# Performance work log

Measured on AMD Instinct MI355X. Metric: run time of the kernel, lower is better.

The kernel has to match this reference:

```python
import jax, jax.numpy as jnp
import numpy as np

N_NODES = 50000
N_EDGES = 800000
IN_DIM, HID, OUT = 128, 64, 64
NUM_REL = 2
LN_EPS = 1e-5


def setup_inputs() -> dict:
    key = jax.random.key(0)
    ks = jax.random.split(key, 16)
    inp = {
        "x": jax.random.normal(ks[0], (N_NODES, IN_DIM), dtype=jnp.float32),
        "edge_index": jax.random.randint(ks[1], (2, N_EDGES), 0, N_NODES, dtype=jnp.int64),
        "edge_type": jax.random.randint(ks[2], (N_EDGES,), 0, NUM_REL, dtype=jnp.int64),
        # layer 1 params (RGCNConv input->hidden + LayerNorm)
        "W1": jax.random.normal(ks[3], (NUM_REL, IN_DIM, HID), dtype=jnp.float32) * 0.05,
        "root1": jax.random.normal(ks[4], (IN_DIM, HID), dtype=jnp.float32) * 0.05,
        "b1": jnp.zeros((HID,), dtype=jnp.float32),
        "g1": jnp.ones((HID,), dtype=jnp.float32),
        "beta1": jnp.zeros((HID,), dtype=jnp.float32),
        # layer 2 params (RGCNConv hidden->output + LayerNorm)
        "W2": jax.random.normal(ks[5], (NUM_REL, HID, OUT), dtype=jnp.float32) * 0.05,
        "root2": jax.random.normal(ks[6], (HID, OUT), dtype=jnp.float32) * 0.05,
        "b2": jnp.zeros((OUT,), dtype=jnp.float32),
        "g2": jnp.ones((OUT,), dtype=jnp.float32),
        "beta2": jnp.zeros((OUT,), dtype=jnp.float32),
    }
    return inp


def rgcn_conv(x, W, root, bias, src, dst, edge_type, num_nodes):
    # PyG RGCNConv (aggr='mean'): out = x @ root + bias + sum_r mean_{j in N_r(i)} x_j @ W_r
    out = x @ root + bias
    for r in range(NUM_REL):
        mask = (edge_type == r).astype(x.dtype)        # [E]
        proj = x @ W[r]                                 # [N, out]
        msg = proj[src] * mask[:, None]                 # [E, out] gather + mask
        agg = jax.ops.segment_sum(msg, dst, num_segments=num_nodes)   # scatter-add
        cnt = jax.ops.segment_sum(mask, dst, num_segments=num_nodes)  # per-relation in-degree
        out = out + agg / jnp.maximum(cnt, 1.0)[:, None]
    return out


def layer_norm(x, g, b):
    mu = jnp.mean(x, axis=-1, keepdims=True)
    var = jnp.mean(jnp.square(x - mu), axis=-1, keepdims=True)
    return (x - mu) * jax.lax.rsqrt(var + LN_EPS) * g + b


def reference(x, edge_index, edge_type, W1, root1, b1, g1, beta1, W2, root2, b2, g2, beta2):
    src, dst = edge_index[0], edge_index[1]
    h = rgcn_conv(x, W1, root1, b1, src, dst, edge_type, x.shape[0])
    h = layer_norm(h, g1, beta1)
    h = jax.nn.gelu(h, approximate=False)  # dropout is identity in eval mode
    h = rgcn_conv(h, W2, root2, b2, src, dst, edge_type, x.shape[0])
    h = layer_norm(h, g2, beta2)
    return h
```

## Files before the change

### kernel.cpp

```cpp
#include <hip/hip_runtime.h>
#include <hip/hip_bf16.h>
#include <math.h>

#define IN_DIM 128
#define HID 64
#define NREL 2

using f32x4 = __attribute__((ext_vector_type(4))) float;
using s16x8 = __attribute__((ext_vector_type(8))) short;

__device__ __forceinline__ short f2bf(float f) {
    unsigned u = __float_as_uint(f);
    unsigned r = (u + 0x7fffu + ((u >> 16) & 1u)) >> 16;
    return (short)r;
}
__device__ __forceinline__ float bf2f(short b) {
    return __uint_as_float(((unsigned)(unsigned short)b) << 16);
}

__global__ void zero_ints(int* p, int n) {
    int i = blockIdx.x * blockDim.x + threadIdx.x;
    if (i < n) p[i] = 0;
}

__global__ void count_edges(const int* __restrict__ et, const int* __restrict__ dst,
                            int* __restrict__ cnt, int E, int N) {
    int e = blockIdx.x * blockDim.x + threadIdx.x;
    if (e < E) {
        atomicAdd(&cnt[et[e] * N + dst[e]], 1);
    }
}

#define SCAN_T 256
#define SCAN_I 4
__global__ void scan_phase1(const int* __restrict__ in, const int* __restrict__ in2,
                            int* __restrict__ excl, int* __restrict__ bsum, int n) {
    __shared__ int sdata[SCAN_T];
    int b = blockIdx.x;
    int t = threadIdx.x;
    int base = b * SCAN_T * SCAN_I;
    int v[SCAN_I];
    int s = 0;
#pragma unroll
    for (int i = 0; i < SCAN_I; ++i) {
        int idx = base + t * SCAN_I + i;
        v[i] = (idx < n) ? (in2 ? in[idx] + in2[idx] : in[idx]) : 0;
        s += v[i];
    }
    sdata[t] = s;
    __syncthreads();
    for (int off = 1; off < SCAN_T; off <<= 1) {
        int x = (t >= off) ? sdata[t - off] : 0;
        __syncthreads();
        sdata[t] += x;
        __syncthreads();
    }
    int run = sdata[t] - s;
    if (bsum && t == SCAN_T - 1) bsum[b] = sdata[SCAN_T - 1];
#pragma unroll
    for (int i = 0; i < SCAN_I; ++i) {
        int idx = base + t * SCAN_I + i;
        if (idx < n) excl[idx] = run;
        run += v[i];
    }
}

__global__ void scan_phase3(const int* __restrict__ excl, const int* __restrict__ boff,
                            int* __restrict__ rowptr, int* __restrict__ cursor,
                            int n, int total) {
    int i = blockIdx.x * blockDim.x + threadIdx.x;
    if (i < n) {
        int v = excl[i] + boff[i / (SCAN_T * SCAN_I)];
        rowptr[i] = v;
        cursor[i] = v;
    }
    if (i == 0) rowptr[n] = total;
}

__global__ void fill_edges(const int* __restrict__ et, const int* __restrict__ src,
                           const int* __restrict__ dst, const int* __restrict__ cnt2,
                           int* __restrict__ cursor, int2* __restrict__ colw,
                           int E, int N) {
    int e = blockIdx.x * blockDim.x + threadIdx.x;
    if (e < E) {
        int d = dst[e];
        int r = et[e];
        int s = src[e];
        int slot = atomicAdd(&cursor[d], 1);
        int deg = cnt2[r * N + d];
        float iw = 1.f / (float)deg;
        unsigned long long v = (unsigned long long)(unsigned)(r * N + s) |
                               ((unsigned long long)__float_as_uint(iw) << 32);
        __hip_atomic_store((unsigned long long*)(colw + slot), v,
                           __ATOMIC_RELAXED, __HIP_MEMORY_SCOPE_AGENT);
    }
}

__device__ __forceinline__ void repack_one(const float* Wa, const float* Wb,
                                           const float* Wr, short* Wf, int T,
                                           int idx) {
    int g = idx >> 9;
    int r = idx & 511;
    int lane = r >> 3;
    int j = r & 7;
    int part = g & 1;
    int ct = g >> 1;
    int t = ct % T;
    int c = ct / T;
    int col = c * 16 + (lane & 15);
    int k = t * 32 + ((lane >> 4) << 3) + j;
    const float* Wg = (col < 64) ? Wa : (col < 128) ? Wb : Wr;
    float v = Wg[(size_t)k * 64 + (col & 63)];
    short hi = f2bf(v);
    Wf[idx] = part ? f2bf(v - bf2f(hi)) : hi;
}

__global__ void repack_w_frag(const float* __restrict__ W1,
                              const float* __restrict__ root1,
                              const float* __restrict__ W2,
                              const float* __restrict__ root2,
                              short* __restrict__ Wf1, short* __restrict__ Wf2) {
    const int L1 = 12 * 4 * 2 * 512;
    const int L2 = 12 * 2 * 2 * 512;
    int tid = blockIdx.x * blockDim.x + threadIdx.x;
    if (tid < L1) {
        repack_one(W1, W1 + (size_t)IN_DIM * 64, root1, Wf1, 4, tid);
    } else if (tid < L1 + L2) {
        repack_one(W2, W2 + (size_t)HID * 64, root2, Wf2, 2, tid - L1);
    }
}

template <int K>
__global__ __launch_bounds__(256) void gemm_mfma(
    const float* __restrict__ X, const short* __restrict__ Wf,
    float* __restrict__ PA, float* __restrict__ PB, float* __restrict__ PR,
    int M) {
    constexpr int T = K / 32;
    const int lane = threadIdx.x & 63;
    const int wid = threadIdx.x >> 6;
    const int row0 = blockIdx.x * 32 + (wid >> 1) * 16;
    const int cbase = (wid & 1) * 6;

    int arow = row0 + (lane & 15);
    if (arow > M - 1) arow = M - 1;
    const float* xr = X + (size_t)arow * K + ((lane >> 4) << 3);
    const s16x8* WfV = (const s16x8*)Wf;

    float4 xa[T][2];
#pragma unroll
    for (int t = 0; t < T; ++t) {
        xa[t][0] = *reinterpret_cast<const float4*>(xr + t * 32);
        xa[t][1] = *reinterpret_cast<const float4*>(xr + t * 32 + 4);
    }
    s16x8 ah[T], al[T];
#pragma unroll
    for (int t = 0; t < T; ++t) {
        const float av[8] = {xa[t][0].x, xa[t][0].y, xa[t][0].z, xa[t][0].w,
                             xa[t][1].x, xa[t][1].y, xa[t][1].z, xa[t][1].w};
#pragma unroll
        for (int j = 0; j < 8; ++j) {
            short h = f2bf(av[j]);
            ah[t][j] = h;
            al[t][j] = f2bf(av[j] - bf2f(h));
        }
    }

    f32x4 acc[6];
#pragma unroll
    for (int c = 0; c < 6; ++c) acc[c] = (f32x4){0.f, 0.f, 0.f, 0.f};

    s16x8 bhA[T], blA[T], bhB[T], blB[T];

#define LOADB(H, L, CG)                                                       \
    {                                                                         \
        _Pragma("unroll") for (int t = 0; t < T; ++t) {                       \
            H[t] = WfV[(size_t)(((CG) * T + t) * 2 + 0) * 64 + lane];         \
            L[t] = WfV[(size_t)(((CG) * T + t) * 2 + 1) * 64 + lane];         \
        }                                                                     \
    }
#define DOMFMA(H, L, CI)                                                      \
    {                                                                         \
        _Pragma("unroll") for (int t = 0; t < T; ++t) {                       \
            acc[CI] = __builtin_amdgcn_mfma_f32_16x16x32_bf16(ah[t], H[t],    \
                                                              acc[CI], 0, 0, 0); \
            acc[CI] = __builtin_amdgcn_mfma_f32_16x16x32_bf16(al[t], H[t],    \
                                                              acc[CI], 0, 0, 0); \
            acc[CI] = __builtin_amdgcn_mfma_f32_16x16x32_bf16(ah[t], L[t],    \
                                                              acc[CI], 0, 0, 0); \
        }                                                                     \
    }

    LOADB(bhA, blA, cbase + 0);
    LOADB(bhB, blB, cbase + 1);
    DOMFMA(bhA, blA, 0);
    LOADB(bhA, blA, cbase + 2);
    DOMFMA(bhB, blB, 1);
    LOADB(bhB, blB, cbase + 3);
    DOMFMA(bhA, blA, 2);
    LOADB(bhA, blA, cbase + 4);
    DOMFMA(bhB, blB, 3);
    LOADB(bhB, blB, cbase + 5);
    DOMFMA(bhA, blA, 4);
    DOMFMA(bhB, blB, 5);

#undef LOADB
#undef DOMFMA

    const int drow = row0 + ((lane >> 4) << 2);
    const int dcol = lane & 15;
#pragma unroll
    for (int ci = 0; ci < 6; ++ci) {
        const int cg = cbase + ci;
        float* base = (cg < 4) ? PA : (cg < 8) ? PB : PR;
        const int cc = (cg & 3) * 16 + dcol;
#pragma unroll
        for (int q = 0; q < 4; ++q) {
            const int row = drow + q;
            if (row < M) base[(size_t)row * 64 + cc] = acc[ci][q];
        }
    }
}

__device__ __forceinline__ float4 shfl_xor_f4(float4 v, int m) {
    return make_float4(__shfl_xor(v.x, m), __shfl_xor(v.y, m),
                       __shfl_xor(v.z, m), __shfl_xor(v.w, m));
}

__global__ __launch_bounds__(256) void agg_ln_kernel(
    const float* __restrict__ Pcat,
    const float* __restrict__ PR,
    const int* __restrict__ rowptr,
    const int2* __restrict__ colw,
    const float* __restrict__ bias, const float* __restrict__ g,
    const float* __restrict__ beta,
    float* __restrict__ out, int N, int gelu) {
    const int t = threadIdx.x;
    const int lane = t & 63;
    const int sub = lane >> 4;
    const int c = lane & 15;
    const int node = blockIdx.x * 4 + (t >> 6);
    if (node >= N) return;

    const int c4 = c * 4;
    float4 acc = *reinterpret_cast<const float4*>(PR + (size_t)node * 64 + c4);
    {
        float4 b4 = *reinterpret_cast<const float4*>(bias + c4);
        acc.x += b4.x; acc.y += b4.y; acc.z += b4.z; acc.w += b4.w;
    }

    const int beg = rowptr[node];
    const int end = rowptr[node + 1];
    float4 s0 = make_float4(0.f, 0.f, 0.f, 0.f);
    float4 s1 = s0, s2 = s0, s3 = s0;
    for (int i = beg + sub; i < end; i += 16) {
        {
            const int2 w = colw[i];
            const float4 v = *reinterpret_cast<const float4*>(Pcat + w.x * 64 + c4);
            const float f = __int_as_float(w.y);
            s0.x = fmaf(v.x, f, s0.x); s0.y = fmaf(v.y, f, s0.y);
            s0.z = fmaf(v.z, f, s0.z); s0.w = fmaf(v.w, f, s0.w);
        }
        int j = i + 4;
        if (j < end) {
            const int2 w = colw[j];
            const float4 v = *reinterpret_cast<const float4*>(Pcat + w.x * 64 + c4);
            const float f = __int_as_float(w.y);
            s1.x = fmaf(v.x, f, s1.x); s1.y = fmaf(v.y, f, s1.y);
            s1.z = fmaf(v.z, f, s1.z); s1.w = fmaf(v.w, f, s1.w);
        }
        j = i + 8;
        if (j < end) {
            const int2 w = colw[j];
            const float4 v = *reinterpret_cast<const float4*>(Pcat + w.x * 64 + c4);
            const float f = __int_as_float(w.y);
            s2.x = fmaf(v.x, f, s2.x); s2.y = fmaf(v.y, f, s2.y);
            s2.z = fmaf(v.z, f, s2.z); s2.w = fmaf(v.w, f, s2.w);
        }
        j = i + 12;
        if (j < end) {
            const int2 w = colw[j];
            const float4 v = *reinterpret_cast<const float4*>(Pcat + w.x * 64 + c4);
            const float f = __int_as_float(w.y);
            s3.x = fmaf(v.x, f, s3.x); s3.y = fmaf(v.y, f, s3.y);
            s3.z = fmaf(v.z, f, s3.z); s3.w = fmaf(v.w, f, s3.w);
        }
    }
    s0.x += s1.x + s2.x + s3.x;
    s0.y += s1.y + s2.y + s3.y;
    s0.z += s1.z + s2.z + s3.z;
    s0.w += s1.w + s2.w + s3.w;
    float4 o = shfl_xor_f4(s0, 16);
    s0.x += o.x; s0.y += o.y; s0.z += o.z; s0.w += o.w;
    o = shfl_xor_f4(s0, 32);
    s0.x += o.x; s0.y += o.y; s0.z += o.z; s0.w += o.w;
    acc.x += s0.x; acc.y += s0.y; acc.z += s0.z; acc.w += s0.w;

    float ps = acc.x + acc.y + acc.z + acc.w;
#pragma unroll
    for (int off = 1; off <= 8; off <<= 1) ps += __shfl_xor(ps, off);
    const float mu = ps * (1.f / 64.f);
    const float4 d = make_float4(acc.x - mu, acc.y - mu, acc.z - mu, acc.w - mu);
    float vs = d.x * d.x + d.y * d.y + d.z * d.z + d.w * d.w;
#pragma unroll
    for (int off = 1; off <= 8; off <<= 1) vs += __shfl_xor(vs, off);
    const float rstd = 1.f / sqrtf(vs * (1.f / 64.f) + 1e-5f);

    const float4 g4 = *reinterpret_cast<const float4*>(g + c4);
    const float4 be4 = *reinterpret_cast<const float4*>(beta + c4);
    float4 y;
    y.x = d.x * rstd * g4.x + be4.x;
    y.y = d.y * rstd * g4.y + be4.y;
    y.z = d.z * rstd * g4.z + be4.z;
    y.w = d.w * rstd * g4.w + be4.w;

    if (gelu) {
        y.x = 0.5f * y.x * (1.f + erff(y.x * 0.70710678118654752440f));
        y.y = 0.5f * y.y * (1.f + erff(y.y * 0.70710678118654752440f));
        y.z = 0.5f * y.z * (1.f + erff(y.z * 0.70710678118654752440f));
        y.w = 0.5f * y.w * (1.f + erff(y.w * 0.70710678118654752440f));
    }

    if (sub == 0)
        *reinterpret_cast<float4*>(out + (size_t)node * 64 + c4) = y;
}

extern "C" void kernel_launch(void* const* d_in, const int* in_sizes, int n_in,
                              void* d_out, int out_size, void* d_ws, size_t ws_size,
                              hipStream_t stream) {
    const float* x = (const float*)d_in[0];
    const int* ei = (const int*)d_in[1];
    const int* et = (const int*)d_in[2];
    const float* W1 = (const float*)d_in[3];
    const float* root1 = (const float*)d_in[4];
    const float* b1 = (const float*)d_in[5];
    const float* g1 = (const float*)d_in[6];
    const float* beta1 = (const float*)d_in[7];
    const float* W2 = (const float*)d_in[8];
    const float* root2 = (const float*)d_in[9];
    const float* b2 = (const float*)d_in[10];
    const float* g2 = (const float*)d_in[11];
    const float* beta2 = (const float*)d_in[12];

    const int E = in_sizes[2];
    const int N = in_sizes[0] / IN_DIM;

    const int WF1 = 12 * 4 * 2 * 512;
    const int WF2 = 12 * 2 * 2 * 512;

    short* Wf1 = (short*)d_ws;
    short* Wf2 = Wf1 + WF1;
    float* Pcat = (float*)(Wf2 + WF2);
    float* PR   = Pcat + (size_t)2 * N * 64;
    float* H    = PR + (size_t)N * 64;
    int2* colw  = (int2*)(H + (size_t)N * 64);
    int* cnt2   = (int*)(colw + E);
    int* excl   = cnt2 + 2 * N;
    int* rowptr = excl + N;
    int* cursor = rowptr + N + 1;
    int* bsum   = cursor + N;
    int* boff   = bsum + 256;

    const int* esrc = ei;
    const int* edst = ei + E;

    zero_ints<<<(2 * N + 255) / 256, 256, 0, stream>>>(cnt2, 2 * N);
    count_edges<<<(E + 255) / 256, 256, 0, stream>>>(et, edst, cnt2, E, N);
    int nb = (N + SCAN_T * SCAN_I - 1) / (SCAN_T * SCAN_I);
    scan_phase1<<<nb, SCAN_T, 0, stream>>>(cnt2, cnt2 + N, excl, bsum, N);
    scan_phase1<<<1, SCAN_T, 0, stream>>>(bsum, nullptr, boff, nullptr, nb);
    scan_phase3<<<(N + 255) / 256, 256, 0, stream>>>(excl, boff, rowptr, cursor, N, E);
    fill_edges<<<(E + 255) / 256, 256, 0, stream>>>(et, esrc, edst, cnt2, cursor,
                                                    colw, E, N);

    repack_w_frag<<<(WF1 + WF2 + 255) / 256, 256, 0, stream>>>(
        W1, root1, W2, root2, Wf1, Wf2);

    int gblocks = (N + 31) / 32;
    gemm_mfma<IN_DIM><<<gblocks, 256, 0, stream>>>(
        x, Wf1, Pcat, Pcat + (size_t)N * 64, PR, N);
    agg_ln_kernel<<<(N + 3) / 4, 256, 0, stream>>>(Pcat, PR, rowptr, colw, b1, g1,
                                                   beta1, H, N, 1);

    gemm_mfma<HID><<<gblocks, 256, 0, stream>>>(
        H, Wf2, Pcat, Pcat + (size_t)N * 64, PR, N);
    agg_ln_kernel<<<(N + 3) / 4, 256, 0, stream>>>(Pcat, PR, rowptr, colw, b2, g2,
                                                   beta2, (float*)d_out, N, 0);
}
```

Measured before the change: 290.3 us.

## Stage weight fragments in LDS and give each wave all 12 output column groups

The GEMM kernel now loads the pre-packed bf16 weight fragments into shared memory in two K-phases. Each wave computes a 16-row tile across all 12 column groups, so each block covers 64 rows instead of 32. Previously each wave read its 6 column groups directly from global memory. The aim is to cut repeated global/L2 weight traffic and halve the block count. In exchange it uses more accumulator registers (12 f32x4), adds LDS staging with barriers, and sets a launch_bounds occupancy hint of 3.

Result: no change. 289.4 us (-0.3%).

```diff
diff --git a/kernel.cpp b/kernel.cpp
--- a/kernel.cpp
+++ b/kernel.cpp
@@ -131,15 +131,18 @@
 }
 
 template <int K>
-__global__ __launch_bounds__(256) void gemm_mfma(
+__global__ __launch_bounds__(256, 3) void gemm_mfma(
     const float* __restrict__ X, const short* __restrict__ Wf,
     float* __restrict__ PA, float* __restrict__ PB, float* __restrict__ PR,
     int M) {
     constexpr int T = K / 32;
-    const int lane = threadIdx.x & 63;
-    const int wid = threadIdx.x >> 6;
-    const int row0 = blockIdx.x * 32 + (wid >> 1) * 16;
-    const int cbase = (wid & 1) * 6;
+    constexpr int TH = T / 2;
+    __shared__ s16x8 WfL[12 * TH * 2 * 64];
+
+    const int tid = threadIdx.x;
+    const int lane = tid & 63;
+    const int wid = tid >> 6;
+    const int row0 = blockIdx.x * 64 + wid * 16;
 
     int arow = row0 + (lane & 15);
     if (arow > M - 1) arow = M - 1;
@@ -165,58 +168,53 @@
         }
     }
 
-    f32x4 acc[6];
-#pragma unroll
-    for (int c = 0; c < 6; ++c) acc[c] = (f32x4){0.f, 0.f, 0.f, 0.f};
-
-    s16x8 bhA[T], blA[T], bhB[T], blB[T];
-
-#define LOADB(H, L, CG)                                                       \
-    {                                                                         \
-        _Pragma("unroll") for (int t = 0; t < T; ++t) {                       \
-            H[t] = WfV[(size_t)(((CG) * T + t) * 2 + 0) * 64 + lane];         \
-            L[t] = WfV[(size_t)(((CG) * T + t) * 2 + 1) * 64 + lane];         \
-        }                                                                     \
-    }
-#define DOMFMA(H, L, CI)                                                      \
-    {                                                                         \
-        _Pragma("unroll") for (int t = 0; t < T; ++t) {                       \
-            acc[CI] = __builtin_amdgcn_mfma_f32_16x16x32_bf16(ah[t], H[t],    \
-                                                              acc[CI], 0, 0, 0); \
-            acc[CI] = __builtin_amdgcn_mfma_f32_16x16x32_bf16(al[t], H[t],    \
-                                                              acc[CI], 0, 0, 0); \
-            acc[CI] = __builtin_amdgcn_mfma_f32_16x16x32_bf16(ah[t], L[t],    \
-                                                              acc[CI], 0, 0, 0); \
-        }                                                                     \
-    }
-
-    LOADB(bhA, blA, cbase + 0);
-    LOADB(bhB, blB, cbase + 1);
-    DOMFMA(bhA, blA, 0);
-    LOADB(bhA, blA, cbase + 2);
-    DOMFMA(bhB, blB, 1);
-    LOADB(bhB, blB, cbase + 3);
-    DOMFMA(bhA, blA, 2);
-    LOADB(bhA, blA, cbase + 4);
-    DOMFMA(bhB, blB, 3);
-    LOADB(bhB, blB, cbase + 5);
-    DOMFMA(bhA, blA, 4);
-    DOMFMA(bhB, blB, 5);
-
-#undef LOADB
-#undef DOMFMA
+    f32x4 acc[12];
+#pragma unroll
+    for (int c = 0; c < 12; ++c) acc[c] = (f32x4){0.f, 0.f, 0.f, 0.f};
+
+#pragma unroll
+    for (int ph = 0; ph < 2; ++ph) {
+        if (ph) __syncthreads();
+#pragma unroll
+        for (int it = 0; it < (12 * TH * 2 * 64) / 256; ++it) {
+            const int v = it * 256 + tid;
+            const int chunk = v >> 6;
+            const int i = v & 63;
+            const int c = chunk / (TH * 2);
+            const int rem = chunk - c * (TH * 2);
+            const int tl = rem >> 1;
+            const int part = rem & 1;
+            const int gsrc = (c * T + ph * TH + tl) * 2 + part;
+            WfL[v] = WfV[(size_t)gsrc * 64 + i];
+        }
+        __syncthreads();
+#pragma unroll
+        for (int c = 0; c < 12; ++c) {
+#pragma unroll
+            for (int tl = 0; tl < TH; ++tl) {
+                const s16x8 bh = WfL[((c * TH + tl) * 2 + 0) * 64 + lane];
+                const s16x8 bl = WfL[((c * TH + tl) * 2 + 1) * 64 + lane];
+                const int tg = ph * TH + tl;
+                acc[c] = __builtin_amdgcn_mfma_f32_16x16x32_bf16(ah[tg], bh,
+                                                                 acc[c], 0, 0, 0);
+                acc[c] = __builtin_amdgcn_mfma_f32_16x16x32_bf16(al[tg], bh,
+                                                                 acc[c], 0, 0, 0);
+                acc[c] = __builtin_amdgcn_mfma_f32_16x16x32_bf16(ah[tg], bl,
+                                                                 acc[c], 0, 0, 0);
+            }
+        }
+    }
 
     const int drow = row0 + ((lane >> 4) << 2);
     const int dcol = lane & 15;
 #pragma unroll
-    for (int ci = 0; ci < 6; ++ci) {
-        const int cg = cbase + ci;
+    for (int cg = 0; cg < 12; ++cg) {
         float* base = (cg < 4) ? PA : (cg < 8) ? PB : PR;
         const int cc = (cg & 3) * 16 + dcol;
 #pragma unroll
         for (int q = 0; q < 4; ++q) {
             const int row = drow + q;
-            if (row < M) base[(size_t)row * 64 + cc] = acc[ci][q];
+            if (row < M) base[(size_t)row * 64 + cc] = acc[cg][q];
         }
     }
 }
@@ -375,7 +373,7 @@
     repack_w_frag<<<(WF1 + WF2 + 255) / 256, 256, 0, stream>>>(
         W1, root1, W2, root2, Wf1, Wf2);
 
-    int gblocks = (N + 31) / 32;
+    int gblocks = (N + 63) / 64;
     gemm_mfma<IN_DIM><<<gblocks, 256, 0, stream>>>(
         x, Wf1, Pcat, Pcat + (size_t)N * 64, PR, N);
     agg_ln_kernel<<<(N + 3) / 4, 256, 0, stream>>>(Pcat, PR, rowptr, colw, b1, g1,
```
